# Kernel tuning notes

Hardware: AMD Instinct MI355X
Metric: run time of the kernel (lower is better)

Reference implementation:

```python
import jax, jax.numpy as jnp
import numpy as np

N = 100000      # nodes
E = 1600000     # edges (before self loops)
M = 40          # n_markers
HID = 128       # hidden
HEADS = 4
DH = HID // HEADS  # 32 per-head dim
LAT = 64
NEG_SLOPE = 0.2
EPS = 1e-5


def setup_inputs() -> dict:
    key = jax.random.key(0)
    ks = jax.random.split(key, 20)
    r = lambda k, shape, s=0.05: (jax.random.normal(k, shape, jnp.float32) * s)
    x = jax.random.normal(ks[0], (N, M), jnp.float32)
    edge_index = jax.random.randint(ks[1], (2, E), 0, N, jnp.int64)
    return {
        "x": x,
        "edge_index": edge_index,
        "Wp": r(ks[2], (M, HID)), "bp": jnp.zeros((HID,), jnp.float32),
        "W1l": r(ks[3], (HID, HID)), "W1r": r(ks[4], (HID, HID)),
        "att1": r(ks[5], (HEADS, DH)), "b1": jnp.zeros((HID,), jnp.float32),
        "W2l": r(ks[6], (HID, HID)), "W2r": r(ks[7], (HID, HID)),
        "att2": r(ks[8], (HEADS, DH)), "b2": jnp.zeros((HID,), jnp.float32),
        "g1": jnp.ones((HID,), jnp.float32), "be1": jnp.zeros((HID,), jnp.float32),
        "g2": jnp.ones((HID,), jnp.float32), "be2": jnp.zeros((HID,), jnp.float32),
        "Wo": r(ks[9], (HID, LAT)), "bo": jnp.zeros((LAT,), jnp.float32),
    }


def _layernorm(z, g, b):
    mu = jnp.mean(z, axis=-1, keepdims=True)
    var = jnp.mean(jnp.square(z - mu), axis=-1, keepdims=True)
    return (z - mu) * jax.lax.rsqrt(var + EPS) * g + b


def _gatv2(h, src, dst, Wl, Wr, att, bias):
    # h: [N, HID]; per-head source/target projections (GATv2, share_weights=False)
    hl = (h @ Wl).reshape(N, HEADS, DH)  # messages (source side)
    hr = (h @ Wr).reshape(N, HEADS, DH)  # target side
    # per-edge attention logits: a^T LeakyReLU(hl[src] + hr[dst])
    e = jax.nn.leaky_relu(hl[src] + hr[dst], NEG_SLOPE)      # [Etot, HEADS, DH]
    logits = jnp.einsum('ehd,hd->eh', e, att)                # [Etot, HEADS]
    # segment softmax over edges sharing the same destination node
    m = jax.ops.segment_max(logits, dst, num_segments=N)     # [N, HEADS]
    ex = jnp.exp(logits - m[dst])
    denom = jax.ops.segment_sum(ex, dst, num_segments=N)     # [N, HEADS]
    alpha = ex / denom[dst]                                  # [Etot, HEADS]
    # scatter-aggregate weighted source messages
    out = jax.ops.segment_sum(hl[src] * alpha[:, :, None], dst, num_segments=N)
    return out.reshape(N, HID) + bias


def reference(x, edge_index, Wp, bp, W1l, W1r, att1, b1, W2l, W2r, att2, b2,
              g1, be1, g2, be2, Wo, bo):
    loops = jnp.arange(N, dtype=edge_index.dtype)
    src = jnp.concatenate([edge_index[0], loops])  # PyG adds self loops by default
    dst = jnp.concatenate([edge_index[1], loops])
    h = x @ Wp + bp
    h = _layernorm(jax.nn.gelu(_gatv2(h, src, dst, W1l, W1r, att1, b1), approximate=False) + h, g1, be1)
    h = _layernorm(jax.nn.gelu(_gatv2(h, src, dst, W2l, W2r, att2, b2), approximate=False) + h, g2, be2)
    return h @ Wo + bo
```

## Files before the change

### kernel.cpp

```cpp
#include <hip/hip_runtime.h>
#include <hip/hip_bf16.h>
#include <math.h>

#define NN   100000
#define EE   1600000
#define ETOT 1700000
#define MM   40
#define HID  128
#define LAT  64
#define NB   391
#define CHUNK 4096

typedef unsigned short u16;
typedef unsigned int   u32;
typedef unsigned long long u64;

typedef __attribute__((ext_vector_type(8))) short bf16x8;
typedef __attribute__((ext_vector_type(4))) float f32x4;
typedef __attribute__((ext_vector_type(2))) float f32x2;

__device__ __forceinline__ float bf2f(u16 a) {
    return __uint_as_float(((u32)a) << 16);
}
__device__ __forceinline__ u16 f2bf(float f) {
    u32 u = __float_as_uint(f);
    u32 r = (u + 0x7fffu + ((u >> 16) & 1u)) >> 16;
    return (u16)r;
}
__device__ __forceinline__ f32x2 unpk(u32 u) {
    f32x2 r;
    r.x = __uint_as_float(u << 16);
    r.y = __uint_as_float(u & 0xffff0000u);
    return r;
}
__device__ __forceinline__ float exp2_hw(float x) {
    float d;
    asm("v_exp_f32 %0, %1" : "=v"(d) : "v"(x));
    return d;
}
__device__ __forceinline__ float gelu_t(float x) {
    float x2 = x * x;
    float y = x * fmaf(0.0713548162726f, x2, 1.59576912161f);
    return x / (1.f + __expf(-y));
}

#define Vbp   0
#define Vatt1 128
#define Vb1   256
#define Vg1   384
#define Vbe1  512
#define Vatt2 640
#define Vb2   768
#define Vg2   896
#define Vbe2  1024
#define Vbo   1152
#define VTOT  1216

#define BWp   0
#define BW1l  8192
#define BW1r  24576
#define BW2l  40960
#define BW2r  57344
#define BWo   73728
#define BTOT  90112

#define NXB   15625
#define NVB   5
#define NWB   352

__device__ __forceinline__ int sniff_bf_wave(const u32* __restrict__ x_raw) {
    int lane = threadIdx.x & 63;
    u32 w = x_raw[lane];
    u16 lo = (u16)(w & 0xffffu);
    int e = (lo >> 7) & 0xFF;
    int ok = (e >= 118 && e <= 133) ? 1 : 0;
    u64 b = __ballot(ok);
    return (__popcll(b) >= 48) ? 1 : 0;
}

__device__ __forceinline__ void edge_decode(const int* __restrict__ ei, int is64, int e,
                                            int& src, int& dst) {
    if (e < EE) {
        src = is64 ? ei[2 * e] : ei[e];
        int idx = EE + e;
        dst = is64 ? ei[2 * idx] : ei[idx];
    } else {
        src = e - EE; dst = src;
    }
}

__global__ __launch_bounds__(256) void prep_kernel(
    const void* __restrict__ x, const u32* __restrict__ ei_raw,
    const void* p0, const void* p1, const void* p2, const void* p3, const void* p4,
    const void* p5, const void* p6, const void* p7, const void* p8, const void* p9,
    const void* w0, const void* w1, const void* w2, const void* w3, const void* w4,
    const void* w5,
    u16* __restrict__ xb, float* __restrict__ wv, u16* __restrict__ wbf,
    int* __restrict__ flags, u32* __restrict__ gbucket, u32* __restrict__ dcnt,
    u32* __restrict__ gcur, u32* __restrict__ dcur)
{
    const u32* x_raw = (const u32*)x;
    int isbf = sniff_bf_wave(x_raw);
    int t = threadIdx.x;
    int b = blockIdx.x;

    if (b == 0) {
        if (t < 64) {
            u32 a = ei_raw[2 * t + 1] | ei_raw[129 + 2 * t];
            u64 nz = __ballot(a != 0u);
            if (t == 0) { flags[0] = (nz == 0uLL) ? 1 : 0; flags[1] = isbf; }
        }
        gbucket[t] = 0; gbucket[t + 256] = 0;
        gcur[t] = 0;    gcur[t + 256] = 0;
        if (t < 64) { dcnt[t] = 0; dcur[t] = 0; }
        return;
    }
    if (b <= NXB) {
        int i = (b - 1) * 256 + t;
        xb[i] = isbf ? ((const u16*)x)[i] : f2bf(((const float*)x)[i]);
        return;
    }
    if (b <= NXB + NVB) {
        int i = (b - 1 - NXB) * 256 + t;
        if (i >= VTOT) return;
        const int offs[11] = {Vbp, Vatt1, Vb1, Vg1, Vbe1, Vatt2, Vb2, Vg2, Vbe2, Vbo, VTOT};
        const void* ps[10] = {p0,p1,p2,p3,p4,p5,p6,p7,p8,p9};
        int s = 0;
#pragma unroll
        for (int k = 1; k < 10; k++) s += (i >= offs[k]) ? 1 : 0;
        int j = i - offs[s];
        const void* p = ps[s];
        wv[i] = isbf ? bf2f(((const u16*)p)[j]) : ((const float*)p)[j];
        return;
    }
    {
        int i = (b - 1 - NXB - NVB) * 256 + t;
        const int offs[7] = {BWp, BW1l, BW1r, BW2l, BW2r, BWo, BTOT};
        const int Ks[6]   = {40, 128, 128, 128, 128, 128};
        const int Ncs[6]  = {128, 128, 128, 128, 128, 64};
        const int Kps[6]  = {64, 128, 128, 128, 128, 128};
        const void* ps[6] = {w0,w1,w2,w3,w4,w5};
        int s = 0;
#pragma unroll
        for (int k = 1; k < 6; k++) s += (i >= offs[k]) ? 1 : 0;
        int j = i - offs[s];
        int Kp = Kps[s];
        int n = j / Kp, k = j % Kp;
        u16 v = 0;
        if (k < Ks[s] && n < Ncs[s]) {
            const void* p = ps[s];
            int src = k * Ncs[s] + n;
            v = isbf ? ((const u16*)p)[src] : f2bf(((const float*)p)[src]);
        }
        wbf[i] = v;
    }
}

__global__ __launch_bounds__(256) void bucket_hist_kernel(
    const int* __restrict__ ei, const int* __restrict__ flags, u32* __restrict__ gbucket)
{
    __shared__ u32 h[512];
    int t = threadIdx.x;
    h[t] = 0; h[t + 256] = 0;
    __syncthreads();
    int is64 = flags[0];
    int base = blockIdx.x * CHUNK;
#pragma unroll
    for (int j = 0; j < CHUNK / 256; j++) {
        int e = base + j * 256 + t;
        if (e < ETOT) {
            int src, dst;
            edge_decode(ei, is64, e, src, dst);
            atomicAdd(&h[dst >> 8], 1u);
        }
    }
    __syncthreads();
    if (h[t])       atomicAdd(&gbucket[t], h[t]);
    if (h[t + 256]) atomicAdd(&gbucket[t + 256], h[t + 256]);
}

__global__ __launch_bounds__(256) void bin_pass_kernel(
    const int* __restrict__ ei, const int* __restrict__ flags,
    const u32* __restrict__ gbucket, u32* __restrict__ gcur, u64* __restrict__ pairs)
{
    __shared__ u32 bh[512];
    __shared__ u32 boff[512];
    __shared__ u32 bbs[512];
    __shared__ u32 bcur[512];
    __shared__ u32 bsc[512];
    __shared__ u64 stage[CHUNK];
    __shared__ u32 ts[256];

    int t = threadIdx.x;
    bh[t] = 0; bh[t + 256] = 0;
    __syncthreads();
    int is64 = flags[0];
    int base = blockIdx.x * CHUNK;
    int chunk_n = ETOT - base; if (chunk_n > CHUNK) chunk_n = CHUNK;

#pragma unroll
    for (int j = 0; j < CHUNK / 256; j++) {
        int e = base + j * 256 + t;
        if (e < ETOT) {
            int src, dst;
            edge_decode(ei, is64, e, src, dst);
            atomicAdd(&bh[dst >> 8], 1u);
        }
    }
    __syncthreads();

    {
        u32 g0v = (2 * t     < NB) ? gbucket[2 * t]     : 0;
        u32 g1v = (2 * t + 1 < NB) ? gbucket[2 * t + 1] : 0;
        u32 ps = g0v + g1v;
        ts[t] = ps; __syncthreads();
        for (int d = 1; d < 256; d <<= 1) {
            u32 v = (t >= d) ? ts[t - d] : 0;
            __syncthreads();
            ts[t] += v;
            __syncthreads();
        }
        u32 ex = ts[t] - ps;
        bsc[2 * t] = ex; bsc[2 * t + 1] = ex + g0v;
    }
    __syncthreads();

    u32 s0 = bh[2 * t], s1 = bh[2 * t + 1];
    u32 tsum = s0 + s1;
    ts[t] = tsum; __syncthreads();
    for (int d = 1; d < 256; d <<= 1) {
        u32 v = (t >= d) ? ts[t - d] : 0;
        __syncthreads();
        ts[t] += v;
        __syncthreads();
    }
    u32 excl = ts[t] - tsum;
    boff[2 * t] = excl; boff[2 * t + 1] = excl + s0;
    bcur[2 * t] = excl; bcur[2 * t + 1] = excl + s0;
    __syncthreads();
    if (t < NB && bh[t]) bbs[t] = bsc[t] + atomicAdd(&gcur[t], bh[t]);
    if (t + 256 < NB && bh[t + 256]) bbs[t + 256] = bsc[t + 256] + atomicAdd(&gcur[t + 256], bh[t + 256]);
    __syncthreads();
#pragma unroll
    for (int j = 0; j < CHUNK / 256; j++) {
        int e = base + j * 256 + t;
        if (e < ETOT) {
            int src, dst;
            edge_decode(ei, is64, e, src, dst);
            u32 pos = atomicAdd(&bcur[dst >> 8], 1u);
            stage[pos] = (u64)src | ((u64)dst << 32);
        }
    }
    __syncthreads();
    for (int i = t; i < chunk_n; i += 256) {
        u64 pr = stage[i];
        u32 b = (u32)(pr >> 32) >> 8;
        pairs[(size_t)bbs[b] + (i - boff[b])] = pr;
    }
}

__global__ __launch_bounds__(256) void sort_pass_kernel(
    const u64* __restrict__ pairs, const u32* __restrict__ gbucket,
    int* __restrict__ srcs, int* __restrict__ offs, u32* __restrict__ dcnt)
{
    __shared__ u32 nh[256];
    __shared__ u32 ns[256];
    __shared__ u32 ncur[256];
    __shared__ u32 dh[64];
    __shared__ u32 bsc[512];
    int t = threadIdx.x;
    int b = blockIdx.x;

    {
        u32 g0v = (2 * t     < NB) ? gbucket[2 * t]     : 0;
        u32 g1v = (2 * t + 1 < NB) ? gbucket[2 * t + 1] : 0;
        u32 ps = g0v + g1v;
        ns[t] = ps; __syncthreads();
        for (int d = 1; d < 256; d <<= 1) {
            u32 v = (t >= d) ? ns[t - d] : 0;
            __syncthreads();
            ns[t] += v;
            __syncthreads();
        }
        u32 ex = ns[t] - ps;
        bsc[2 * t] = ex; bsc[2 * t + 1] = ex + g0v;
    }
    __syncthreads();
    u32 beg = bsc[b], endp = bsc[b + 1];

    nh[t] = 0;
    if (t < 64) dh[t] = 0;
    __syncthreads();
    for (u32 i = beg + t; i < endp; i += 256) {
        u32 dst = (u32)(pairs[i] >> 32);
        atomicAdd(&nh[dst & 255], 1u);
    }
    __syncthreads();
    u32 cnt = nh[t];
    ns[t] = cnt; __syncthreads();
    for (int d = 1; d < 256; d <<= 1) {
        u32 v = (t >= d) ? ns[t - d] : 0;
        __syncthreads();
        ns[t] += v;
        __syncthreads();
    }
    u32 excl = ns[t] - cnt;
    int id = b * 256 + t;
    if (id <= NN) offs[id] = (int)(beg + excl);
    if (id < NN) atomicAdd(&dh[cnt < 63u ? cnt : 63u], 1u);
    ncur[t] = excl;
    __syncthreads();
    if (t < 64 && dh[t]) atomicAdd(&dcnt[t], dh[t]);
    for (u32 i = beg + t; i < endp; i += 256) {
        u64 pr = pairs[i];
        u32 loc = ((u32)(pr >> 32)) & 255;
        u32 p = atomicAdd(&ncur[loc], 1u);
        srcs[beg + p] = (int)(u32)pr;
    }
}

__global__ __launch_bounds__(256) void deg_perm_kernel(
    const int* __restrict__ offs, const u32* __restrict__ dcnt,
    u32* __restrict__ dcur, int* __restrict__ perm)
{
    __shared__ u32 cnt[64];
    __shared__ u32 base[64];
    __shared__ u32 sb[64];
    int t = threadIdx.x;
    if (t < 64) {
        u32 v = dcnt[t];
        u32 x = v;
#pragma unroll
        for (int off = 1; off < 64; off <<= 1) {
            u32 y = __shfl_down(x, off);
            if (t + off < 64) x += y;
        }
        sb[t] = x - v;
        cnt[t] = 0;
    }
    __syncthreads();
    int i = blockIdx.x * 256 + t;
    int d = 0; u32 r = 0;
    bool ok = (i < NN);
    if (ok) {
        d = offs[i + 1] - offs[i];
        if (d > 63) d = 63;
        r = atomicAdd(&cnt[d], 1u);
    }
    __syncthreads();
    if (t < 64 && cnt[t]) base[t] = sb[t] + atomicAdd(&dcur[t], cnt[t]);
    __syncthreads();
    if (ok) perm[base[d] + r] = i;
}

__global__ __launch_bounds__(256) void mfma_gemm(
    const u16* __restrict__ A, int lda,
    const u16* __restrict__ Bt, int ldb,
    const float* __restrict__ bias,
    int nrows, int ksteps, int ncols,
    float* __restrict__ outF, u16* __restrict__ outB, u16* __restrict__ outB2, int ldo,
    int mode, const int* __restrict__ flags)
{
    int lane = threadIdx.x & 63;
    int wv = threadIdx.x >> 6;
    int wx = wv & 1, wy = wv >> 1;
    int l16 = lane & 15, quad = lane >> 4;
    int r0 = blockIdx.x * 128 + wx * 64;
    int n0 = wy * 64;

    Bt += (size_t)blockIdx.y * 128 * ldb;
    if (blockIdx.y) outB = outB2;

    f32x4 acc[4][4];
#pragma unroll
    for (int m = 0; m < 4; m++)
#pragma unroll
        for (int n = 0; n < 4; n++) acc[m][n] = (f32x4){0.f, 0.f, 0.f, 0.f};

    const u16* Ap = A + (size_t)(r0 + l16) * lda + quad * 8;
    const u16* Bp = Bt + (size_t)(n0 + l16) * ldb + quad * 8;

    for (int k = 0; k < ksteps; ++k) {
        bf16x8 af[4], bfr[4];
#pragma unroll
        for (int m = 0; m < 4; m++)
            af[m] = *(const bf16x8*)(Ap + (size_t)m * 16 * lda + k * 32);
#pragma unroll
        for (int n = 0; n < 4; n++)
            bfr[n] = *(const bf16x8*)(Bp + (size_t)n * 16 * ldb + k * 32);
#pragma unroll
        for (int m = 0; m < 4; m++)
#pragma unroll
            for (int n = 0; n < 4; n++)
                acc[m][n] = __builtin_amdgcn_mfma_f32_16x16x32_bf16(af[m], bfr[n], acc[m][n], 0, 0, 0);
    }

    int mk = mode;
    if (mk < 0) mk = flags[1] ? 2 : 1;

#pragma unroll
    for (int m = 0; m < 4; m++) {
#pragma unroll
        for (int n = 0; n < 4; n++) {
            int col = n0 + n * 16 + l16;
            float bb = (bias != nullptr && col < ncols) ? bias[col] : 0.f;
#pragma unroll
            for (int reg = 0; reg < 4; reg++) {
                int row = r0 + m * 16 + quad * 4 + reg;
                if (row < nrows && col < ncols) {
                    float v = acc[m][n][reg] + bb;
                    if (mk & 1) outF[(size_t)row * ldo + col] = v;
                    if (mk & 2) outB[(size_t)row * ldo + col] = f2bf(v);
                }
            }
        }
    }
}

__global__ __launch_bounds__(256) void gat_agg_kernel(
    const u16* __restrict__ hl, const u16* __restrict__ hr, const u16* __restrict__ hresb,
    const float* __restrict__ att, const float* __restrict__ bias,
    const float* __restrict__ gamma, const float* __restrict__ beta,
    const int* __restrict__ offs, const int* __restrict__ srcs,
    const int* __restrict__ perm,
    u16* __restrict__ outb)
{
    int lane = threadIdx.x & 63;
    int sub = lane >> 4;
    int r = lane & 15;
    int c0 = r * 8;
    u32 cb = (u32)(r << 4);
    int id = (blockIdx.x * 4 + (threadIdx.x >> 6)) * 4 + sub;
    int dst = perm[id];

    int start = offs[dst];
    int deg = offs[dst + 1] - start;
    int dm = deg - 1;
    const char* hlc = (const char*)hl;

    f32x2 hr2[4], av2[4];
    {
        uint4 q = *(const uint4*)((const char*)hr + ((u32)dst << 8) + cb);
        hr2[0] = unpk(q.x); hr2[1] = unpk(q.y); hr2[2] = unpk(q.z); hr2[3] = unpk(q.w);
        const float L2E = 1.4426950408889634f;
        float4 a0 = *(const float4*)&att[c0];
        float4 a1 = *(const float4*)&att[c0 + 4];
        av2[0] = (f32x2){L2E * a0.x, L2E * a0.y}; av2[1] = (f32x2){L2E * a0.z, L2E * a0.w};
        av2[2] = (f32x2){L2E * a1.x, L2E * a1.y}; av2[3] = (f32x2){L2E * a1.z, L2E * a1.w};
    }

    int md = deg;
    md = max(md, __shfl_xor(md, 16));
    md = max(md, __shfl_xor(md, 32));

    f32x2 acc2[4];
#pragma unroll
    for (int i = 0; i < 4; i++) acc2[i] = (f32x2){0.f, 0.f};
    float s = 0.f;

    int sa = srcs[start];
    int sb = srcs[start + (1 < dm ? 1 : dm)];
    uint4 qa = *(const uint4*)(hlc + ((u32)sa << 8) + cb);
    uint4 qb = *(const uint4*)(hlc + ((u32)sb << 8) + cb);
    int sna = srcs[start + (2 < dm ? 2 : dm)];
    int snb = srcs[start + (3 < dm ? 3 : dm)];

    int mi = (md + 1) >> 1;
    for (int j = 0; j < mi; ++j) {
        int e4 = 2 * j + 4, e5 = 2 * j + 5;
        int sna2 = srcs[start + min(e4, dm)];
        int snb2 = srcs[start + min(e5, dm)];
        uint4 qna = *(const uint4*)(hlc + ((u32)sna << 8) + cb);
        uint4 qnb = *(const uint4*)(hlc + ((u32)snb << 8) + cb);

        f32x2 ha[4], hb[4];
        ha[0] = unpk(qa.x); ha[1] = unpk(qa.y); ha[2] = unpk(qa.z); ha[3] = unpk(qa.w);
        hb[0] = unpk(qb.x); hb[1] = unpk(qb.y); hb[2] = unpk(qb.z); hb[3] = unpk(qb.w);
        f32x2 pa2 = (f32x2){0.f, 0.f};
        f32x2 pb2 = (f32x2){0.f, 0.f};
#pragma unroll
        for (int i = 0; i < 4; i++) {
            f32x2 za = ha[i] + hr2[i];
            f32x2 zb = hb[i] + hr2[i];
            f32x2 la = __builtin_elementwise_max(za, za * 0.2f);
            f32x2 lb = __builtin_elementwise_max(zb, zb * 0.2f);
            pa2 = __builtin_elementwise_fma(av2[i], la, pa2);
            pb2 = __builtin_elementwise_fma(av2[i], lb, pb2);
        }
        float pa = pa2.x + pa2.y;
        float pb = pb2.x + pb2.y;
        pa += __shfl_xor(pa, 1); pb += __shfl_xor(pb, 1);
        pa += __shfl_xor(pa, 2); pb += __shfl_xor(pb, 2);
        int e0 = 2 * j, e1 = 2 * j + 1;
        float wa = (e0 < deg) ? exp2_hw(pa) : 0.f;
        float wb = (e1 < deg) ? exp2_hw(pb) : 0.f;
        s += wa + wb;
        f32x2 wa2 = (f32x2){wa, wa};
        f32x2 wb2 = (f32x2){wb, wb};
#pragma unroll
        for (int i = 0; i < 4; i++)
            acc2[i] = __builtin_elementwise_fma(wa2, ha[i],
                      __builtin_elementwise_fma(wb2, hb[i], acc2[i]));

        qa = qna; qb = qnb; sna = sna2; snb = snb2;
    }

    float inv = 1.f / s;
    float v[8];
    {
        float4 b0 = *(const float4*)&bias[c0];
        float4 b1 = *(const float4*)&bias[c0 + 4];
        float bb[8] = {b0.x,b0.y,b0.z,b0.w,b1.x,b1.y,b1.z,b1.w};
        uint4 qr = *(const uint4*)((const char*)hresb + ((u32)dst << 8) + cb);
        f32x2 rr2[4] = {unpk(qr.x), unpk(qr.y), unpk(qr.z), unpk(qr.w)};
#pragma unroll
        for (int i = 0; i < 4; i++) {
            float t0 = fmaf(acc2[i].x, inv, bb[2*i]);
            float t1 = fmaf(acc2[i].y, inv, bb[2*i+1]);
            v[2*i]   = gelu_t(t0) + rr2[i].x;
            v[2*i+1] = gelu_t(t1) + rr2[i].y;
        }
    }

    float s1 = 0.f, s2 = 0.f;
#pragma unroll
    for (int k = 0; k < 8; k++) { s1 += v[k]; s2 = fmaf(v[k], v[k], s2); }
#pragma unroll
    for (int off = 1; off < 16; off <<= 1) {
        s1 += __shfl_xor(s1, off);
        s2 += __shfl_xor(s2, off);
    }
    float mu  = s1 * (1.f / 128.f);
    float var = s2 * (1.f / 128.f) - mu * mu;
    float rstd = rsqrtf(var + 1e-5f);

    float4 g0 = *(const float4*)&gamma[c0];
    float4 g1 = *(const float4*)&gamma[c0 + 4];
    float4 be0 = *(const float4*)&beta[c0];
    float4 be1 = *(const float4*)&beta[c0 + 4];
    float gg[8] = {g0.x,g0.y,g0.z,g0.w,g1.x,g1.y,g1.z,g1.w};
    float eb[8] = {be0.x,be0.y,be0.z,be0.w,be1.x,be1.y,be1.z,be1.w};
    float o[8];
#pragma unroll
    for (int k = 0; k < 8; k++) o[k] = fmaf((v[k] - mu) * rstd, gg[k], eb[k]);
    uint4 pk;
    pk.x = (u32)f2bf(o[0]) | ((u32)f2bf(o[1]) << 16);
    pk.y = (u32)f2bf(o[2]) | ((u32)f2bf(o[3]) << 16);
    pk.z = (u32)f2bf(o[4]) | ((u32)f2bf(o[5]) << 16);
    pk.w = (u32)f2bf(o[6]) | ((u32)f2bf(o[7]) << 16);
    *(uint4*)((char*)outb + ((u32)dst << 8) + cb) = pk;
}

extern "C" void kernel_launch(void* const* d_in, const int* in_sizes, int n_in,
                              void* d_out, int out_size, void* d_ws, size_t ws_size,
                              hipStream_t stream) {
    const void* x  = d_in[0];
    const int*  ei = (const int*)d_in[1];

    char* ws = (char*)d_ws;
    size_t off = 0;
    auto alloc = [&](size_t bytes) -> void* {
        void* p = ws + off;
        off = (off + bytes + 511) & ~(size_t)511;
        return p;
    };
    u16*   xb      = (u16*)  alloc(((size_t)NN * MM + 8192) * 2);
    float* wv      = (float*)alloc((size_t)VTOT * 4);
    u16*   wbf     = (u16*)  alloc((size_t)BTOT * 2);
    u16*   h0b     = (u16*)  alloc((size_t)(NN + 64) * HID * 2);
    u16*   h1b     = (u16*)  alloc((size_t)(NN + 64) * HID * 2);
    u16*   hlb     = (u16*)  alloc((size_t)NN * HID * 2);
    u16*   hrb     = (u16*)  alloc((size_t)NN * HID * 2);
    int*   offs    = (int*)  alloc((size_t)(NN + 1) * 4);
    u32*   gbucket = (u32*)  alloc(512 * 4);
    u32*   gcur    = (u32*)  alloc(512 * 4);
    int*   flags   = (int*)  alloc(512);
    int*   srcs    = (int*)  alloc(((size_t)ETOT + 64) * 4);
    u64*   pairs   = (u64*)  alloc((size_t)ETOT * 8);
    u32*   dcnt    = (u32*)  alloc(64 * 4);
    u32*   dcur    = (u32*)  alloc(64 * 4);
    int*   perm    = (int*)  alloc((size_t)NN * 4);

    prep_kernel<<<1 + NXB + NVB + NWB, 256, 0, stream>>>(
        x, (const u32*)ei,
        d_in[3], d_in[6], d_in[7], d_in[12], d_in[13], d_in[10], d_in[11], d_in[14], d_in[15], d_in[17],
        d_in[2], d_in[4], d_in[5], d_in[8], d_in[9], d_in[16],
        xb, wv, wbf, flags, gbucket, dcnt, gcur, dcur);

    const int EB = (ETOT + CHUNK - 1) / CHUNK;
    bucket_hist_kernel<<<EB, 256, 0, stream>>>(ei, flags, gbucket);
    bin_pass_kernel<<<EB, 256, 0, stream>>>(ei, flags, gbucket, gcur, pairs);
    sort_pass_kernel<<<NB, 256, 0, stream>>>(pairs, gbucket, srcs, offs, dcnt);

    deg_perm_kernel<<<NB, 256, 0, stream>>>(offs, dcnt, dcur, perm);

    const int GB = (NN + 127) / 128;
    const int AB = NN / 16;

    mfma_gemm<<<dim3(GB, 1), 256, 0, stream>>>(xb, MM, wbf + BWp, 64, wv + Vbp,
                                               NN, 2, HID, nullptr, h0b, nullptr, HID, 2, flags);

    mfma_gemm<<<dim3(GB, 2), 256, 0, stream>>>(h0b, HID, wbf + BW1l, HID, nullptr,
                                               NN, 4, HID, nullptr, hlb, hrb, HID, 2, flags);
    gat_agg_kernel<<<AB, 256, 0, stream>>>(hlb, hrb, h0b, wv + Vatt1, wv + Vb1,
                                           wv + Vg1, wv + Vbe1, offs, srcs, perm, h1b);

    mfma_gemm<<<dim3(GB, 2), 256, 0, stream>>>(h1b, HID, wbf + BW2l, HID, nullptr,
                                               NN, 4, HID, nullptr, hlb, hrb, HID, 2, flags);
    gat_agg_kernel<<<AB, 256, 0, stream>>>(hlb, hrb, h1b, wv + Vatt2, wv + Vb2,
                                           wv + Vg2, wv + Vbe2, offs, srcs, perm, h0b);

    mfma_gemm<<<dim3(GB, 1), 256, 0, stream>>>(h0b, HID, wbf + BWo, HID, wv + Vbo,
                                               NN, 4, LAT, (float*)d_out, (u16*)d_out, nullptr, LAT, -1, flags);
}
```

Before: 474.1 us.

## Add specialized 64-row layer GEMM with async LDS A-tile load

Replaces the generic MFMA GEMM used for the two per-layer projections with a dedicated kernel. Each block loads one 64x128 A tile into LDS once, using global_load_lds with an XOR swizzle to avoid bank conflicts. Each of its four waves then computes 64 output columns, so the Wl and Wr outputs come from one pass over A instead of separate y-blocks. The hl/hr buffers are padded to NN+64 rows. The kernel relies on the B matrix being laid out as a transposed, concatenated 256x128 array.

```diff
diff --git a/kernel.cpp b/kernel.cpp
--- a/kernel.cpp
+++ b/kernel.cpp
@@ -37,6 +37,11 @@
     float d;
     asm("v_exp_f32 %0, %1" : "=v"(d) : "v"(x));
     return d;
+}
+__device__ __forceinline__ void gload_lds16(const void* g, void* l) {
+    __builtin_amdgcn_global_load_lds(
+        (const __attribute__((address_space(1))) void*)g,
+        (__attribute__((address_space(3))) void*)l, 16, 0, 0);
 }
 __device__ __forceinline__ float gelu_t(float x) {
     float x2 = x * x;
@@ -412,6 +417,79 @@
                     if (mk & 1) outF[(size_t)row * ldo + col] = v;
                     if (mk & 2) outB[(size_t)row * ldo + col] = f2bf(v);
                 }
+            }
+        }
+    }
+}
+
+__global__ __launch_bounds__(256) void gemm_layer(
+    const u16* __restrict__ A,
+    const u16* __restrict__ Bt,
+    u16* __restrict__ outL, u16* __restrict__ outR)
+{
+    __shared__ u16 Atile[64 * 128];
+    int t = threadIdx.x;
+    int wv = t >> 6, lane = t & 63;
+    int l16 = lane & 15, quad = lane >> 4;
+    int r0 = blockIdx.x * 64;
+
+    {
+        const char* Ab = (const char*)(A + (size_t)r0 * 128);
+        char* Lb = (char*)Atile + wv * 4096;
+        u32 baseP = (u32)(wv * 4096) + (u32)lane * 16;
+#pragma unroll
+        for (int j = 0; j < 4; j++) {
+            u32 P = baseP + (u32)(j * 1024);
+            u32 row = P >> 8;
+            u32 L = P ^ ((row & 7u) << 4);
+            gload_lds16(Ab + L, Lb + j * 1024);
+        }
+    }
+
+    f32x4 acc[4][4];
+#pragma unroll
+    for (int m = 0; m < 4; m++)
+#pragma unroll
+        for (int n = 0; n < 4; n++) acc[m][n] = (f32x4){0.f, 0.f, 0.f, 0.f};
+
+    int n0 = wv * 64;
+    const u16* Bp = Bt + (size_t)(n0 + l16) * 128 + quad * 8;
+    const char* At = (const char*)Atile;
+
+    __syncthreads();
+
+#pragma unroll
+    for (int k = 0; k < 4; k++) {
+        bf16x8 af[4], bfr[4];
+#pragma unroll
+        for (int n = 0; n < 4; n++)
+            bfr[n] = *(const bf16x8*)(Bp + (size_t)n * 16 * 128 + k * 32);
+#pragma unroll
+        for (int m = 0; m < 4; m++) {
+            u32 arow = (u32)(m * 16 + l16);
+            u32 Lb = arow * 256 + (u32)(quad * 16 + k * 64);
+            u32 Pb = Lb ^ ((arow & 7u) << 4);
+            af[m] = *(const bf16x8*)(At + Pb);
+        }
+#pragma unroll
+        for (int m = 0; m < 4; m++)
+#pragma unroll
+            for (int n = 0; n < 4; n++)
+                acc[m][n] = __builtin_amdgcn_mfma_f32_16x16x32_bf16(af[m], bfr[n], acc[m][n], 0, 0, 0);
+    }
+
+    u16* outp = (wv < 2) ? outL : outR;
+    int nb = n0 & 127;
+#pragma unroll
+    for (int m = 0; m < 4; m++) {
+#pragma unroll
+        for (int n = 0; n < 4; n++) {
+            int col = nb + n * 16 + l16;
+#pragma unroll
+            for (int reg = 0; reg < 4; reg++) {
+                int row = r0 + m * 16 + quad * 4 + reg;
+                if (row < NN)
+                    outp[(size_t)row * 128 + col] = f2bf(acc[m][n][reg]);
             }
         }
     }
@@ -569,8 +647,8 @@
     u16*   wbf     = (u16*)  alloc((size_t)BTOT * 2);
     u16*   h0b     = (u16*)  alloc((size_t)(NN + 64) * HID * 2);
     u16*   h1b     = (u16*)  alloc((size_t)(NN + 64) * HID * 2);
-    u16*   hlb     = (u16*)  alloc((size_t)NN * HID * 2);
-    u16*   hrb     = (u16*)  alloc((size_t)NN * HID * 2);
+    u16*   hlb     = (u16*)  alloc((size_t)(NN + 64) * HID * 2);
+    u16*   hrb     = (u16*)  alloc((size_t)(NN + 64) * HID * 2);
     int*   offs    = (int*)  alloc((size_t)(NN + 1) * 4);
     u32*   gbucket = (u32*)  alloc(512 * 4);
     u32*   gcur    = (u32*)  alloc(512 * 4);
@@ -595,18 +673,17 @@
     deg_perm_kernel<<<NB, 256, 0, stream>>>(offs, dcnt, dcur, perm);
 
     const int GB = (NN + 127) / 128;
+    const int LB = (NN + 63) / 64;
     const int AB = NN / 16;
 
     mfma_gemm<<<dim3(GB, 1), 256, 0, stream>>>(xb, MM, wbf + BWp, 64, wv + Vbp,
                                                NN, 2, HID, nullptr, h0b, nullptr, HID, 2, flags);
 
-    mfma_gemm<<<dim3(GB, 2), 256, 0, stream>>>(h0b, HID, wbf + BW1l, HID, nullptr,
-                                               NN, 4, HID, nullptr, hlb, hrb, HID, 2, flags);
+    gemm_layer<<<LB, 256, 0, stream>>>(h0b, wbf + BW1l, hlb, hrb);
     gat_agg_kernel<<<AB, 256, 0, stream>>>(hlb, hrb, h0b, wv + Vatt1, wv + Vb1,
                                            wv + Vg1, wv + Vbe1, offs, srcs, perm, h1b);
 
-    mfma_gemm<<<dim3(GB, 2), 256, 0, stream>>>(h1b, HID, wbf + BW2l, HID, nullptr,
-                                               NN, 4, HID, nullptr, hlb, hrb, HID, 2, flags);
+    gemm_layer<<<LB, 256, 0, stream>>>(h1b, wbf + BW2l, hlb, hrb);
     gat_agg_kernel<<<AB, 256, 0, stream>>>(hlb, hrb, h1b, wv + Vatt2, wv + Vb2,
                                            wv + Vg2, wv + Vbe2, offs, srcs, perm, h0b);
 
```

Result: faster. 419.2 us (-11.6%).
